# Kernel optimization log

Measured on AMD Instinct MI355X. Metric: run time of the kernel, lower is better.

## Reference

```python
import jax, jax.numpy as jnp
import numpy as np

TEMPERATURE = 0.5
EPS = 1e-8  # torch CosineSimilarity eps


def _simclr_loss(z_i, z_j):
    # z_i, z_j: [B, T, F]
    B, T, F = z_i.shape
    N = 2 * B
    # z[t] = cat(z_i[:, t], z_j[:, t]) -> [T, N, F]
    z = jnp.swapaxes(jnp.concatenate([z_i, z_j], axis=0), 0, 1)
    # Cosine similarity via normalize + matmul (instead of NxNxF broadcast)
    norm = jnp.maximum(jnp.linalg.norm(z, axis=-1, keepdims=True), EPS)
    zn = z / norm
    sim = jnp.einsum('tnf,tmf->tnm', zn, zn) / TEMPERATURE  # [T, N, N]
    # positives: sim[t, i, i+B] and sim[t, i+B, i]
    pos = jnp.concatenate(
        [jnp.diagonal(sim, offset=B, axis1=1, axis2=2),
         jnp.diagonal(sim, offset=-B, axis1=1, axis2=2)], axis=1)  # [T, N]
    # CE with label 0 on [pos, negatives] == logsumexp(row w/o diagonal) - pos
    # (the candidate set {pos} U negatives is exactly the row minus its diagonal)
    diag = jnp.eye(N, dtype=bool)
    masked = jnp.where(diag, -jnp.inf, sim)
    lse = jax.scipy.special.logsumexp(masked, axis=-1)  # [T, N]
    # per-t loss is sum over N rows / N; total is mean over T
    return jnp.mean(jnp.sum(lse - pos, axis=-1) / N)


def setup_inputs() -> dict:
    key = jax.random.key(0)
    k1, k2 = jax.random.split(key)
    B, T, F = 128, 256, 512
    z_i = jax.random.normal(k1, (B, T, F), dtype=jnp.float32)
    z_j = jax.random.normal(k2, (B, T, F), dtype=jnp.float32)
    return {"z_i": z_i, "z_j": z_j}


def reference(z_i, z_j):
    return _simclr_loss(z_i, z_j)
```

## Files before the change

kernel.cpp:

```cpp
#include <hip/hip_runtime.h>
#include <hip/hip_bf16.h>


#define Bc 128
#define Tc 256
#define Fc 512
#define Nc 256
#define BK 64

typedef __bf16 bf16x8 __attribute__((ext_vector_type(8)));
typedef float f32x4 __attribute__((ext_vector_type(4)));

__global__ __launch_bounds__(512, 2)
void simclr_fused(const float* __restrict__ zi, const float* __restrict__ zj,
                  float* __restrict__ out) {
  const int t    = blockIdx.x;
  const int tid  = threadIdx.x;
  const int lane = tid & 63;
  const int wid  = tid >> 6;
  const int wr   = wid & 3;
  const int wc   = wid >> 2;

  __shared__ __align__(16) __bf16 tile[2][Nc * BK];
  __shared__ float rowssq[Nc];
  __shared__ float invn[Nc];
  __shared__ float rowsum[Nc];
  __shared__ float posv[Nc];
  __shared__ float wsum[8];

  if (tid < Nc) rowsum[tid] = 0.f;
  __syncthreads();

  const float* srow[4];
  int ssl[4], wof[4];
#pragma unroll
  for (int j = 0; j < 4; ++j) {
    int g   = tid + j * 512;
    int row = g >> 3;
    int s   = g & 7;
    ssl[j]  = s;
    wof[j]  = (row << 6) + ((s ^ (row & 7)) << 3);
    srow[j] = (row < Bc) ? (zi + ((size_t)row * Tc + t) * Fc)
                         : (zj + ((size_t)(row - Bc) * Tc + t) * Fc);
  }

  f32x4 acc[4][8];
#pragma unroll
  for (int m = 0; m < 4; ++m)
#pragma unroll
    for (int n = 0; n < 8; ++n)
      acc[m][n] = (f32x4){0.f, 0.f, 0.f, 0.f};

  float4 ra[4], rb[4];

  auto LOADR = [&](int kt) {
#pragma unroll
    for (int j = 0; j < 4; ++j) {
      const float4* p = reinterpret_cast<const float4*>(srow[j] + kt * BK + ssl[j] * 8);
      ra[j] = p[0];
      rb[j] = p[1];
    }
  };
  auto WRITE = [&](int b) {
#pragma unroll
    for (int j = 0; j < 4; ++j) {
      bf16x8 v;
      v[0]=(__bf16)ra[j].x; v[1]=(__bf16)ra[j].y; v[2]=(__bf16)ra[j].z; v[3]=(__bf16)ra[j].w;
      v[4]=(__bf16)rb[j].x; v[5]=(__bf16)rb[j].y; v[6]=(__bf16)rb[j].z; v[7]=(__bf16)rb[j].w;
      *reinterpret_cast<bf16x8*>(&tile[b][wof[j]]) = v;
    }
  };

  LOADR(0);
  WRITE(0);

  for (int kt = 0; kt < 8; ++kt) {
    __syncthreads();
    if (kt < 7) LOADR(kt + 1);
    const __bf16* tb = tile[kt & 1];
#pragma unroll
    for (int kk = 0; kk < 2; ++kk) {
      const int kslot = (kk << 2) + (lane >> 4);
      bf16x8 bfrag[8];
#pragma unroll
      for (int n = 0; n < 8; ++n) {
        int c  = (wc << 7) + (n << 4) + (lane & 15);
        int sw = kslot ^ (c & 7);
        bfrag[n] = *reinterpret_cast<const bf16x8*>(&tb[(c << 6) + (sw << 3)]);
      }
#pragma unroll
      for (int m = 0; m < 4; ++m) {
        int r  = (wr << 6) + (m << 4) + (lane & 15);
        int sw = kslot ^ (r & 7);
        bf16x8 afrag = *reinterpret_cast<const bf16x8*>(&tb[(r << 6) + (sw << 3)]);
#pragma unroll
        for (int n = 0; n < 8; ++n)
          acc[m][n] = __builtin_amdgcn_mfma_f32_16x16x32_bf16(afrag, bfrag[n],
                                                              acc[m][n], 0, 0, 0);
      }
    }
    if (kt < 7) WRITE((kt + 1) & 1);
  }

#pragma unroll
  for (int m = 0; m < 4; ++m)
#pragma unroll
    for (int q = 0; q < 4; ++q) {
      int r = (wr << 6) + (m << 4) + ((lane >> 4) << 2) + q;
#pragma unroll
      for (int n = 0; n < 8; ++n) {
        int c = (wc << 7) + (n << 4) + (lane & 15);
        if (c == r) rowssq[r] = acc[m][n][q];
      }
    }
  __syncthreads();
  if (tid < Nc) invn[tid] = 1.0f / fmaxf(sqrtf(rowssq[tid]), 1e-8f);
  __syncthreads();

#pragma unroll
  for (int m = 0; m < 4; ++m) {
#pragma unroll
    for (int q = 0; q < 4; ++q) {
      int r = (wr << 6) + (m << 4) + ((lane >> 4) << 2) + q;
      float inr = invn[r];
      float partial = 0.f;
#pragma unroll
      for (int n = 0; n < 8; ++n) {
        int c = (wc << 7) + (n << 4) + (lane & 15);
        float s = acc[m][n][q] * inr * invn[c] * 2.0f;
        if (c == (r ^ Bc)) posv[r] = s;
        if (c != r) partial += __expf(s);
      }
      partial += __shfl_xor(partial, 1);
      partial += __shfl_xor(partial, 2);
      partial += __shfl_xor(partial, 4);
      partial += __shfl_xor(partial, 8);
      if ((lane & 15) == 0) atomicAdd(&rowsum[r], partial);
    }
  }

  __syncthreads();
  float v = 0.f;
  if (tid < Nc) v = __logf(rowsum[tid]) - posv[tid];
#pragma unroll
  for (int off = 32; off > 0; off >>= 1) v += __shfl_down(v, off);
  if (lane == 0) wsum[wid] = v;
  __syncthreads();
  if (tid == 0) {
    float sum = 0.f;
#pragma unroll
    for (int i = 0; i < 8; ++i) sum += wsum[i];
    atomicAdd(out, sum * (1.0f / 65536.0f));
  }
}

extern "C" void kernel_launch(void* const* d_in, const int* in_sizes, int n_in,
                              void* d_out, int out_size, void* d_ws, size_t ws_size,
                              hipStream_t stream) {
  const float* zi = (const float*)d_in[0];
  const float* zj = (const float*)d_in[1];
  float* out = (float*)d_out;
  hipMemsetAsync(out, 0, sizeof(float) * out_size, stream);
  simclr_fused<<<Tc, 512, 0, stream>>>(zi, zj, out);
}
```

Measured before the change: 156.2 us.

## Double block to 1024 threads with 64x64 per-wave tiles and row-coalesced loads

New measurement: 152.6 us. 1.02x faster.

```diff
diff --git a/kernel.cpp b/kernel.cpp
--- a/kernel.cpp
+++ b/kernel.cpp
@@ -7,11 +7,13 @@
 #define Fc 512
 #define Nc 256
 #define BK 64
+#define NW 16
 
 typedef __bf16 bf16x8 __attribute__((ext_vector_type(8)));
+typedef __bf16 bf16x4 __attribute__((ext_vector_type(4)));
 typedef float f32x4 __attribute__((ext_vector_type(4)));
 
-__global__ __launch_bounds__(512, 2)
+__global__ __launch_bounds__(1024, 4)
 void simclr_fused(const float* __restrict__ zi, const float* __restrict__ zj,
                   float* __restrict__ out) {
   const int t    = blockIdx.x;
@@ -26,76 +28,74 @@
   __shared__ float invn[Nc];
   __shared__ float rowsum[Nc];
   __shared__ float posv[Nc];
-  __shared__ float wsum[8];
+  __shared__ float wsum[NW];
 
   if (tid < Nc) rowsum[tid] = 0.f;
-  __syncthreads();
 
-  const float* srow[4];
-  int ssl[4], wof[4];
+  const float* sp[4];
 #pragma unroll
   for (int j = 0; j < 4; ++j) {
-    int g   = tid + j * 512;
-    int row = g >> 3;
-    int s   = g & 7;
-    ssl[j]  = s;
-    wof[j]  = (row << 6) + ((s ^ (row & 7)) << 3);
-    srow[j] = (row < Bc) ? (zi + ((size_t)row * Tc + t) * Fc)
-                         : (zj + ((size_t)(row - Bc) * Tc + t) * Fc);
+    int row = (wid << 4) + (j << 2) + (lane >> 4);
+    const float* base = (row < Bc) ? (zi + ((size_t)row * Tc + t) * Fc)
+                                   : (zj + ((size_t)(row - Bc) * Tc + t) * Fc);
+    sp[j] = base + ((lane & 15) << 2);
+  }
+  int wof2[2];
+#pragma unroll
+  for (int j = 0; j < 2; ++j) {
+    int row = (wid << 4) + (j << 2) + (lane >> 4);
+    int s = (lane & 15) >> 1;
+    wof2[j] = (row << 7) + (((s ^ (row & 7)) << 4) | ((lane & 1) << 3));
   }
 
-  f32x4 acc[4][8];
+  f32x4 acc[4][4];
 #pragma unroll
   for (int m = 0; m < 4; ++m)
 #pragma unroll
-    for (int n = 0; n < 8; ++n)
+    for (int n = 0; n < 4; ++n)
       acc[m][n] = (f32x4){0.f, 0.f, 0.f, 0.f};
 
-  float4 ra[4], rb[4];
+  float4 ra[4];
 
   auto LOADR = [&](int kt) {
 #pragma unroll
-    for (int j = 0; j < 4; ++j) {
-      const float4* p = reinterpret_cast<const float4*>(srow[j] + kt * BK + ssl[j] * 8);
-      ra[j] = p[0];
-      rb[j] = p[1];
-    }
+    for (int j = 0; j < 4; ++j)
+      ra[j] = *reinterpret_cast<const float4*>(sp[j] + kt * BK);
   };
   auto WRITE = [&](int b) {
+    char* tb = (char*)&tile[b][0];
 #pragma unroll
     for (int j = 0; j < 4; ++j) {
-      bf16x8 v;
-      v[0]=(__bf16)ra[j].x; v[1]=(__bf16)ra[j].y; v[2]=(__bf16)ra[j].z; v[3]=(__bf16)ra[j].w;
-      v[4]=(__bf16)rb[j].x; v[5]=(__bf16)rb[j].y; v[6]=(__bf16)rb[j].z; v[7]=(__bf16)rb[j].w;
-      *reinterpret_cast<bf16x8*>(&tile[b][wof[j]]) = v;
+      bf16x4 v;
+      v[0] = (__bf16)ra[j].x; v[1] = (__bf16)ra[j].y;
+      v[2] = (__bf16)ra[j].z; v[3] = (__bf16)ra[j].w;
+      *reinterpret_cast<bf16x4*>(tb + wof2[j & 1] + (j >> 1) * 1024) = v;
     }
   };
 
+  __syncthreads();
   LOADR(0);
   WRITE(0);
 
   for (int kt = 0; kt < 8; ++kt) {
     __syncthreads();
     if (kt < 7) LOADR(kt + 1);
-    const __bf16* tb = tile[kt & 1];
+    const char* tb = (const char*)&tile[kt & 1][0];
 #pragma unroll
     for (int kk = 0; kk < 2; ++kk) {
-      const int kslot = (kk << 2) + (lane >> 4);
-      bf16x8 bfrag[8];
+      const int sws = ((kk << 2) + (lane >> 4)) ^ (lane & 7);
+      const char* ab = tb + ((((wr << 6) + (lane & 15)) << 7) + (sws << 4));
+      const char* bb = tb + ((((wc << 6) + (lane & 15)) << 7) + (sws << 4));
+      bf16x8 bf[4];
 #pragma unroll
-      for (int n = 0; n < 8; ++n) {
-        int c  = (wc << 7) + (n << 4) + (lane & 15);
-        int sw = kslot ^ (c & 7);
-        bfrag[n] = *reinterpret_cast<const bf16x8*>(&tb[(c << 6) + (sw << 3)]);
-      }
+      for (int n = 0; n < 4; ++n)
+        bf[n] = *reinterpret_cast<const bf16x8*>(bb + (n << 11));
 #pragma unroll
       for (int m = 0; m < 4; ++m) {
-        int r  = (wr << 6) + (m << 4) + (lane & 15);
-        int sw = kslot ^ (r & 7);
-        bf16x8 afrag = *reinterpret_cast<const bf16x8*>(&tb[(r << 6) + (sw << 3)]);
+        bf16x8 af = *reinterpret_cast<const bf16x8*>(ab + (m << 11));
 #pragma unroll
-        for (int n = 0; n < 8; ++n)
-          acc[m][n] = __builtin_amdgcn_mfma_f32_16x16x32_bf16(afrag, bfrag[n],
+        for (int n = 0; n < 4; ++n)
+          acc[m][n] = __builtin_amdgcn_mfma_f32_16x16x32_bf16(af, bf[n],
                                                               acc[m][n], 0, 0, 0);
       }
     }
@@ -108,8 +108,8 @@
     for (int q = 0; q < 4; ++q) {
       int r = (wr << 6) + (m << 4) + ((lane >> 4) << 2) + q;
 #pragma unroll
-      for (int n = 0; n < 8; ++n) {
-        int c = (wc << 7) + (n << 4) + (lane & 15);
+      for (int n = 0; n < 4; ++n) {
+        int c = (wc << 6) + (n << 4) + (lane & 15);
         if (c == r) rowssq[r] = acc[m][n][q];
       }
     }
@@ -125,8 +125,8 @@
       float inr = invn[r];
       float partial = 0.f;
 #pragma unroll
-      for (int n = 0; n < 8; ++n) {
-        int c = (wc << 7) + (n << 4) + (lane & 15);
+      for (int n = 0; n < 4; ++n) {
+        int c = (wc << 6) + (n << 4) + (lane & 15);
         float s = acc[m][n][q] * inr * invn[c] * 2.0f;
         if (c == (r ^ Bc)) posv[r] = s;
         if (c != r) partial += __expf(s);
@@ -149,7 +149,7 @@
   if (tid == 0) {
     float sum = 0.f;
 #pragma unroll
-    for (int i = 0; i < 8; ++i) sum += wsum[i];
+    for (int i = 0; i < NW; ++i) sum += wsum[i];
     atomicAdd(out, sum * (1.0f / 65536.0f));
   }
 }
@@ -161,5 +161,5 @@
   const float* zj = (const float*)d_in[1];
   float* out = (float*)d_out;
   hipMemsetAsync(out, 0, sizeof(float) * out_size, stream);
-  simclr_fused<<<Tc, 512, 0, stream>>>(zi, zj, out);
+  simclr_fused<<<Tc, 1024, 0, stream>>>(zi, zj, out);
 }
```
